# Performance work log

Measured on AMD Instinct MI355X. Metric: run time of the kernel, lower is better.

Reference implementation:

```python
import jax, jax.numpy as jnp
import numpy as np

N_HEADS = 16

def setup_inputs() -> dict:
    key = jax.random.key(0)
    ks = jax.random.split(key, 5)
    d = 2048
    s = 0.02
    return {
        "x": jax.random.normal(ks[0], (1, 2048, d), dtype=jnp.float32),
        "Wq": jax.random.normal(ks[1], (d, d), dtype=jnp.float32) * s,
        "bq": jnp.zeros((d,), jnp.float32),
        "Wk": jax.random.normal(ks[2], (d, d), dtype=jnp.float32) * s,
        "bk": jnp.zeros((d,), jnp.float32),
        "Wv": jax.random.normal(ks[3], (d, d), dtype=jnp.float32) * s,
        "bv": jnp.zeros((d,), jnp.float32),
        "Wo": jax.random.normal(ks[4], (d, d), dtype=jnp.float32) * s,
        "bo": jnp.zeros((d,), jnp.float32),
    }

def reference(x, Wq, bq, Wk, bk, Wv, bv, Wo, bo):
    B, S, D = x.shape
    H = N_HEADS
    dk = D // H
    # QKV projections -> [B, H, S, dk]
    def proj(W, b):
        return (x @ W + b).reshape(B, S, H, dk).transpose(0, 2, 1, 3)
    q, k, v = proj(Wq, bq), proj(Wk, bk), proj(Wv, bv)
    scores = jnp.einsum('bhqd,bhkd->bhqk', q, k) / jnp.sqrt(jnp.float32(dk))
    # _apply_sliding_window_attention: block-reshaped tril == plain causal mask
    causal = jnp.tril(jnp.ones((S, S), dtype=bool))
    scores = jnp.where(causal, scores, -jnp.inf)
    probs = jax.nn.softmax(scores, axis=-1)
    out = jnp.einsum('bhqk,bhkd->bhqd', probs, v)  # [B,H,S,dk]
    out = out.transpose(0, 2, 1, 3).reshape(B, S, D)
    return out @ Wo + bo
```

## Files before the change

kernel.cpp:

```cpp
#include <hip/hip_runtime.h>
#include <stdint.h>

typedef unsigned short u16;
typedef __attribute__((ext_vector_type(8))) __bf16 bf16x8;
typedef __attribute__((ext_vector_type(4))) float f32x4;

#define LOG2E 1.4426950408889634f

__device__ __forceinline__ u16 f2bf(float f) {
  union { float f; uint32_t u; } v; v.f = f;
  uint32_t r = v.u + 0x7fffu + ((v.u >> 16) & 1u);
  return (u16)(r >> 16);
}

__device__ __forceinline__ float bf2f(u16 u) {
  union { uint32_t u; float f; } v; v.u = ((uint32_t)u) << 16;
  return v.f;
}

__device__ __forceinline__ void gl_lds16(const void* g, void* l) {
  __builtin_amdgcn_global_load_lds((const __attribute__((address_space(1))) void*)g,
                                   (__attribute__((address_space(3))) void*)l,
                                   16, 0, 0);
}

__device__ __forceinline__ f32x4 mfma16(bf16x8 a, bf16x8 b, f32x4 c) {
  return __builtin_amdgcn_mfma_f32_16x16x32_bf16(a, b, c, 0, 0, 0);
}

__global__ void cvt_bf16(const float* __restrict__ src, u16* __restrict__ dst) {
  int i = (blockIdx.x * 256 + threadIdx.x) * 4;
  float4 f = *(const float4*)(src + i);
  ushort4 o;
  o.x = f2bf(f.x); o.y = f2bf(f.y); o.z = f2bf(f.z); o.w = f2bf(f.w);
  *(ushort4*)(dst + i) = o;
}

__global__ void transpose_cvt(const float* __restrict__ W0, const float* __restrict__ W1,
                              const float* __restrict__ W2, const float* __restrict__ W3,
                              u16* __restrict__ out) {
  __shared__ float tile[64][65];
  int z = blockIdx.z;
  const float* W = (z == 0) ? W0 : (z == 1) ? W1 : (z == 2) ? W2 : W3;
  u16* dst = out + (size_t)z * 2048 * 2048;
  int k0 = blockIdx.y * 64, n0 = blockIdx.x * 64;
  int lx = threadIdx.x & 63, ly = threadIdx.x >> 6;
#pragma unroll
  for (int p = 0; p < 16; ++p) {
    int row = p * 4 + ly;
    tile[row][lx] = W[(size_t)(k0 + row) * 2048 + n0 + lx];
  }
  __syncthreads();
#pragma unroll
  for (int p = 0; p < 16; ++p) {
    int row = p * 4 + ly;
    dst[(size_t)(n0 + row) * 2048 + k0 + lx] = f2bf(tile[lx][row]);
  }
}

__launch_bounds__(256, 2)
__global__ void gemm_bt(const u16* __restrict__ A, const u16* __restrict__ Bt,
                        int mode,
                        const float* __restrict__ b0, const float* __restrict__ b1,
                        const float* __restrict__ b2,
                        float* __restrict__ outF, u16* __restrict__ outQ,
                        u16* __restrict__ outK, u16* __restrict__ outVT) {
  extern __shared__ char smem[];
  u16* As = (u16*)smem;
  u16* Bs = (u16*)(smem + 16384);
  const int K = 2048;
  const int tid = threadIdx.x;
  const int lane = tid & 63, wid = tid >> 6;
  const int c = lane & 15, q = lane >> 4;
  const int wm = wid >> 1, wn = wid & 1;
  const int tm = blockIdx.y, tn = blockIdx.x;
  const size_t Abase = (size_t)tm * 128 * K;
  const size_t Bbase = (size_t)tn * 128 * K;

  f32x4 acc[4][4] = {};

  for (int kt = 0; kt < K / 64; ++kt) {
#pragma unroll
    for (int t = 0; t < 4; ++t) {
      int slot = wid * 256 + t * 64 + lane;
      int row = slot >> 3, cs = slot & 7;
      int cc = cs ^ (row & 7);
      const u16* ga = A + Abase + (size_t)row * K + kt * 64 + cc * 8;
      gl_lds16(ga, (char*)As + (size_t)(wid * 256 + t * 64) * 16);
      const u16* gb = Bt + Bbase + (size_t)row * K + kt * 64 + cc * 8;
      gl_lds16(gb, (char*)Bs + (size_t)(wid * 256 + t * 64) * 16);
    }
    __syncthreads();
#pragma unroll
    for (int kc = 0; kc < 2; ++kc) {
      bf16x8 af[4], bfr[4];
#pragma unroll
      for (int i = 0; i < 4; ++i) {
        int rowa = wm * 64 + i * 16 + c;
        int cha = ((kc << 2) | q) ^ (rowa & 7);
        af[i] = *(const bf16x8*)((const char*)As + rowa * 128 + cha * 16);
        int rowb = wn * 64 + i * 16 + c;
        int chb = ((kc << 2) | q) ^ (rowb & 7);
        bfr[i] = *(const bf16x8*)((const char*)Bs + rowb * 128 + chb * 16);
      }
#pragma unroll
      for (int i = 0; i < 4; ++i)
#pragma unroll
        for (int j = 0; j < 4; ++j)
          acc[i][j] = mfma16(af[i], bfr[j], acc[i][j]);
    }
    __syncthreads();
  }

  if (mode == 0) {
#pragma unroll
    for (int i = 0; i < 4; ++i) {
      int rowg = tm * 128 + wm * 64 + i * 16 + q * 4;
#pragma unroll
      for (int j = 0; j < 4; ++j) {
        int colg = tn * 128 + wn * 64 + j * 16 + c;
        float bias = b0[colg];
#pragma unroll
        for (int r = 0; r < 4; ++r)
          outF[(size_t)(rowg + r) * 2048 + colg] = acc[i][j][r] + bias;
      }
    }
  } else {
    int proj = tn >> 4;
    int h = tn & 15;
    const float* bias = (proj == 0) ? b0 : (proj == 1) ? b1 : b2;
    if (proj < 2) {
      u16* out = (proj == 0) ? outQ : outK;
      float scale = (proj == 0) ? 0.08838834764831845f : 1.0f;
#pragma unroll
      for (int i = 0; i < 4; ++i) {
        int s0 = tm * 128 + wm * 64 + i * 16 + q * 4;
#pragma unroll
        for (int j = 0; j < 4; ++j) {
          int d = wn * 64 + j * 16 + c;
          float bv = bias[h * 128 + d];
#pragma unroll
          for (int r = 0; r < 4; ++r) {
            float v = (acc[i][j][r] + bv) * scale;
            out[((size_t)h * 2048 + s0 + r) * 128 + d] = f2bf(v);
          }
        }
      }
    } else {
      u16* Cs = (u16*)smem;
#pragma unroll
      for (int i = 0; i < 4; ++i) {
        int sl = wm * 64 + i * 16 + q * 4;
#pragma unroll
        for (int j = 0; j < 4; ++j) {
          int dl = wn * 64 + j * 16 + c;
          float bv = bias[h * 128 + dl];
          ushort4 pk;
          pk.x = f2bf(acc[i][j][0] + bv);
          pk.y = f2bf(acc[i][j][1] + bv);
          pk.z = f2bf(acc[i][j][2] + bv);
          pk.w = f2bf(acc[i][j][3] + bv);
          *(ushort4*)(Cs + dl * 136 + sl) = pk;
        }
      }
      __syncthreads();
#pragma unroll
      for (int rr = 0; rr < 8; ++rr) {
        int d = rr * 16 + (tid >> 4);
        int sc = (tid & 15) * 8;
        uint4 vv = *(const uint4*)(Cs + d * 136 + sc);
        *(uint4*)(outVT + ((size_t)(h * 128 + d)) * 2048 + tm * 128 + sc) = vv;
      }
    }
  }
}

__launch_bounds__(256, 2)
__global__ void attn_kernel(const u16* __restrict__ Qb, const u16* __restrict__ Kb,
                            const u16* __restrict__ Vt,
                            u16* __restrict__ Op0, u16* __restrict__ Op1,
                            float* __restrict__ lp0, float* __restrict__ lp1) {
  extern __shared__ char smem[];
  u16* Ks = (u16*)smem;
  u16* Vs = (u16*)(smem + 16384);
  u16* Ps = (u16*)(smem + 32768);
  int b = blockIdx.x;
  int split, qt, h;
  if (b < 256) { split = 0; qt = b >> 4; h = b & 15; }
  else { split = 1; int idx = b - 256; qt = 15 - (idx >> 4); h = idx & 15; }
  u16* Op = split ? Op1 : Op0;
  float* lp = split ? lp1 : lp0;
  const int ktBase = split ? (qt + 1) : 0;
  const int ntiles = qt + 1;

  const int tid = threadIdx.x, lane = tid & 63, wid = tid >> 6;
  const int c = lane & 15, q = lane >> 4;

  bf16x8 qf[2][4];
#pragma unroll
  for (int i = 0; i < 2; ++i) {
    int s = qt * 128 + wid * 32 + i * 16 + c;
    const u16* qrow = Qb + ((size_t)h * 2048 + s) * 128;
#pragma unroll
    for (int kc = 0; kc < 4; ++kc)
      qf[i][kc] = *(const bf16x8*)(qrow + kc * 32 + q * 8);
  }

  f32x4 oacc[2][8] = {};
  float lst[2][4] = {};

  for (int tt = 0; tt < ntiles; ++tt) {
    const int kt = ktBase + tt;
    if (tt) __syncthreads();
#pragma unroll
    for (int t = 0; t < 4; ++t) {
      int slot = (wid * 4 + t) * 64 + lane;
      int rowk = slot >> 4, csk = slot & 15;
      int cck = csk ^ (rowk & 7);
      const u16* gk = Kb + ((size_t)h * 2048 + kt * 64 + rowk) * 128 + cck * 8;
      gl_lds16(gk, (char*)Ks + (size_t)((wid * 4 + t) * 64) * 16);
      int rowv = slot >> 3, csv = slot & 7;
      int ccv = csv ^ (rowv & 7);
      const u16* gv = Vt + ((size_t)(h * 128 + rowv)) * 2048 + kt * 64 + ccv * 8;
      gl_lds16(gv, (char*)Vs + (size_t)((wid * 4 + t) * 64) * 16);
    }
    __syncthreads();

    f32x4 sacc[2][4] = {};
#pragma unroll
    for (int kc = 0; kc < 4; ++kc) {
      bf16x8 bfr[4];
#pragma unroll
      for (int j = 0; j < 4; ++j) {
        int row = j * 16 + c;
        int ch = ((kc << 2) | q) ^ (row & 7);
        bfr[j] = *(const bf16x8*)((const char*)Ks + row * 256 + ch * 16);
      }
#pragma unroll
      for (int i = 0; i < 2; ++i)
#pragma unroll
        for (int j = 0; j < 4; ++j)
          sacc[i][j] = mfma16(qf[i][kc], bfr[j], sacc[i][j]);
    }

    if (kt >= 2 * qt) {
#pragma unroll
      for (int i = 0; i < 2; ++i)
#pragma unroll
        for (int j = 0; j < 4; ++j) {
          int key = kt * 64 + j * 16 + c;
#pragma unroll
          for (int r = 0; r < 4; ++r) {
            int qrow = qt * 128 + wid * 32 + i * 16 + q * 4 + r;
            if (key > qrow) sacc[i][j][r] = -1e30f;
          }
        }
    }

#pragma unroll
    for (int i = 0; i < 2; ++i)
#pragma unroll
      for (int j = 0; j < 4; ++j)
#pragma unroll
        for (int r = 0; r < 4; ++r) {
          float p = __builtin_amdgcn_exp2f(sacc[i][j][r] * LOG2E);
          sacc[i][j][r] = p;
          lst[i][r] += p;
        }

#pragma unroll
    for (int i = 0; i < 2; ++i)
#pragma unroll
      for (int j = 0; j < 4; ++j)
#pragma unroll
        for (int r = 0; r < 4; ++r)
          Ps[wid * 2304 + (i * 16 + q * 4 + r) * 72 + j * 16 + c] = f2bf(sacc[i][j][r]);

#pragma unroll
    for (int kc = 0; kc < 2; ++kc) {
      bf16x8 af[2], bv[8];
#pragma unroll
      for (int i = 0; i < 2; ++i)
        af[i] = *(const bf16x8*)((const char*)Ps + wid * 4608 + (i * 16 + c) * 144 +
                                 kc * 64 + q * 16);
#pragma unroll
      for (int jo = 0; jo < 8; ++jo) {
        int row = jo * 16 + c;
        int ch = ((kc << 2) | q) ^ (row & 7);
        bv[jo] = *(const bf16x8*)((const char*)Vs + row * 128 + ch * 16);
      }
#pragma unroll
      for (int i = 0; i < 2; ++i)
#pragma unroll
        for (int jo = 0; jo < 8; ++jo)
          oacc[i][jo] = mfma16(af[i], bv[jo], oacc[i][jo]);
    }
  }

#pragma unroll
  for (int i = 0; i < 2; ++i) {
#pragma unroll
    for (int r = 0; r < 4; ++r) {
      float l = lst[i][r];
      l += __shfl_xor(l, 1);
      l += __shfl_xor(l, 2);
      l += __shfl_xor(l, 4);
      l += __shfl_xor(l, 8);
      lst[i][r] = l;
      int s = qt * 128 + wid * 32 + i * 16 + q * 4 + r;
      if (c == 0) lp[(size_t)h * 2048 + s] = l;
    }
#pragma unroll
    for (int jo = 0; jo < 8; ++jo) {
#pragma unroll
      for (int r = 0; r < 4; ++r) {
        int s = qt * 128 + wid * 32 + i * 16 + q * 4 + r;
        Op[((size_t)h * 2048 + s) * 128 + jo * 16 + c] = f2bf(oacc[i][jo][r]);
      }
    }
  }
}

__global__ void attn_combine(const u16* __restrict__ Op0, const u16* __restrict__ Op1,
                             const float* __restrict__ lp0, const float* __restrict__ lp1,
                             u16* __restrict__ AO) {
  int g = blockIdx.x * 256 + threadIdx.x;
  int row = g >> 4;
  int dd = (g & 15) * 8;
  int h = row >> 11, s = row & 2047;
  float inv = 1.0f / (lp0[row] + lp1[row]);
  uint4 a = *(const uint4*)(Op0 + (size_t)row * 128 + dd);
  uint4 bb = *(const uint4*)(Op1 + (size_t)row * 128 + dd);
  const u16* pa = (const u16*)&a;
  const u16* pb = (const u16*)&bb;
  u16 res[8];
#pragma unroll
  for (int t = 0; t < 8; ++t)
    res[t] = f2bf((bf2f(pa[t]) + bf2f(pb[t])) * inv);
  *(uint4*)(AO + (size_t)s * 2048 + h * 128 + dd) = *(uint4*)res;
}

extern "C" void kernel_launch(void* const* d_in, const int* in_sizes, int n_in,
                              void* d_out, int out_size, void* d_ws, size_t ws_size,
                              hipStream_t stream) {
  const float* x  = (const float*)d_in[0];
  const float* Wq = (const float*)d_in[1];
  const float* bq = (const float*)d_in[2];
  const float* Wk = (const float*)d_in[3];
  const float* bk = (const float*)d_in[4];
  const float* Wv = (const float*)d_in[5];
  const float* bv = (const float*)d_in[6];
  const float* Wo = (const float*)d_in[7];
  const float* bo = (const float*)d_in[8];

  char* ws = (char*)d_ws;
  u16* xb = (u16*)(ws);
  u16* wt = (u16*)(ws + (size_t)8  * 1048576);
  u16* Qb = (u16*)(ws + (size_t)40 * 1048576);
  u16* Kb = (u16*)(ws + (size_t)48 * 1048576);
  u16* Vt = (u16*)(ws + (size_t)56 * 1048576);
  u16* AO = (u16*)(ws + (size_t)64 * 1048576);
  u16* Op0 = (u16*)(ws);
  u16* Op1 = (u16*)(ws + (size_t)8 * 1048576);
  float* l0 = (float*)(ws + (size_t)16 * 1048576);
  float* l1 = (float*)(ws + (size_t)16 * 1048576 + 131072);

  cvt_bf16<<<4096, 256, 0, stream>>>(x, xb);
  transpose_cvt<<<dim3(32, 32, 4), 256, 0, stream>>>(Wq, Wk, Wv, Wo, wt);
  gemm_bt<<<dim3(48, 16), 256, 34816, stream>>>(xb, wt, 1, bq, bk, bv,
                                                nullptr, Qb, Kb, Vt);
  attn_kernel<<<512, 256, 51200, stream>>>(Qb, Kb, Vt, Op0, Op1, l0, l1);
  attn_combine<<<2048, 256, 0, stream>>>(Op0, Op1, l0, l1, AO);
  gemm_bt<<<dim3(16, 16), 256, 34816, stream>>>(AO, wt + (size_t)3 * 2048 * 2048, 0,
                                                bo, nullptr, nullptr,
                                                (float*)d_out, nullptr, nullptr, nullptr);
}
```

Before: 264.4 us.

## Use packed bf16 conversion, vectorize stores, transpose PV MFMA, raise attention occupancy

Replaces the manual round-to-nearest bf16 conversion with the HIP packed float2-to-bfloat162 intrinsic, which can lower to a hardware packed-convert instruction on gfx950. Stores in the conversion, transpose and combine kernels are widened to 8- or 16-byte writes. In the attention kernel, the MFMA operands for the PV product are swapped so each lane holds four consecutive head-dim outputs, and the output is written as 8-byte vector stores. The attention kernel's launch bound is raised from 2 to 3 blocks per CU, which may force register spills.

```diff
diff --git a/kernel.cpp b/kernel.cpp
--- a/kernel.cpp
+++ b/kernel.cpp
@@ -1,4 +1,5 @@
 #include <hip/hip_runtime.h>
+#include <hip/hip_bf16.h>
 #include <stdint.h>
 
 typedef unsigned short u16;
@@ -7,15 +8,15 @@
 
 #define LOG2E 1.4426950408889634f
 
-__device__ __forceinline__ u16 f2bf(float f) {
-  union { float f; uint32_t u; } v; v.f = f;
-  uint32_t r = v.u + 0x7fffu + ((v.u >> 16) & 1u);
-  return (u16)(r >> 16);
-}
-
 __device__ __forceinline__ float bf2f(u16 u) {
   union { uint32_t u; float f; } v; v.u = ((uint32_t)u) << 16;
   return v.f;
+}
+
+__device__ __forceinline__ uint32_t pk2(float a, float b) {
+  union { __hip_bfloat162 h; uint32_t u; } x;
+  x.h = __float22bfloat162_rn(make_float2(a, b));
+  return x.u;
 }
 
 __device__ __forceinline__ void gl_lds16(const void* g, void* l) {
@@ -31,9 +32,10 @@
 __global__ void cvt_bf16(const float* __restrict__ src, u16* __restrict__ dst) {
   int i = (blockIdx.x * 256 + threadIdx.x) * 4;
   float4 f = *(const float4*)(src + i);
-  ushort4 o;
-  o.x = f2bf(f.x); o.y = f2bf(f.y); o.z = f2bf(f.z); o.w = f2bf(f.w);
-  *(ushort4*)(dst + i) = o;
+  uint2 o;
+  o.x = pk2(f.x, f.y);
+  o.y = pk2(f.z, f.w);
+  *(uint2*)(dst + i) = o;
 }
 
 __global__ void transpose_cvt(const float* __restrict__ W0, const float* __restrict__ W1,
@@ -51,10 +53,17 @@
     tile[row][lx] = W[(size_t)(k0 + row) * 2048 + n0 + lx];
   }
   __syncthreads();
-#pragma unroll
-  for (int p = 0; p < 16; ++p) {
-    int row = p * 4 + ly;
-    dst[(size_t)(n0 + row) * 2048 + k0 + lx] = f2bf(tile[lx][row]);
+  int kc = threadIdx.x & 7;
+  int rbase = threadIdx.x >> 3;
+#pragma unroll
+  for (int p = 0; p < 2; ++p) {
+    int n = rbase + p * 32;
+    uint4 o;
+    o.x = pk2(tile[kc * 8 + 0][n], tile[kc * 8 + 1][n]);
+    o.y = pk2(tile[kc * 8 + 2][n], tile[kc * 8 + 3][n]);
+    o.z = pk2(tile[kc * 8 + 4][n], tile[kc * 8 + 5][n]);
+    o.w = pk2(tile[kc * 8 + 6][n], tile[kc * 8 + 7][n]);
+    *(uint4*)(dst + (size_t)(n0 + n) * 2048 + k0 + kc * 8) = o;
   }
 }
 
@@ -139,11 +148,13 @@
         for (int j = 0; j < 4; ++j) {
           int d = wn * 64 + j * 16 + c;
           float bv = bias[h * 128 + d];
-#pragma unroll
-          for (int r = 0; r < 4; ++r) {
-            float v = (acc[i][j][r] + bv) * scale;
-            out[((size_t)h * 2048 + s0 + r) * 128 + d] = f2bf(v);
-          }
+          uint32_t p01 = pk2((acc[i][j][0] + bv) * scale, (acc[i][j][1] + bv) * scale);
+          uint32_t p23 = pk2((acc[i][j][2] + bv) * scale, (acc[i][j][3] + bv) * scale);
+          u16* o = out + ((size_t)h * 2048 + s0) * 128 + d;
+          o[0]       = (u16)p01;
+          o[128]     = (u16)(p01 >> 16);
+          o[256]     = (u16)p23;
+          o[384]     = (u16)(p23 >> 16);
         }
       }
     } else {
@@ -155,12 +166,10 @@
         for (int j = 0; j < 4; ++j) {
           int dl = wn * 64 + j * 16 + c;
           float bv = bias[h * 128 + dl];
-          ushort4 pk;
-          pk.x = f2bf(acc[i][j][0] + bv);
-          pk.y = f2bf(acc[i][j][1] + bv);
-          pk.z = f2bf(acc[i][j][2] + bv);
-          pk.w = f2bf(acc[i][j][3] + bv);
-          *(ushort4*)(Cs + dl * 136 + sl) = pk;
+          uint2 pk;
+          pk.x = pk2(acc[i][j][0] + bv, acc[i][j][1] + bv);
+          pk.y = pk2(acc[i][j][2] + bv, acc[i][j][3] + bv);
+          *(uint2*)(Cs + dl * 136 + sl) = pk;
         }
       }
       __syncthreads();
@@ -175,7 +184,7 @@
   }
 }
 
-__launch_bounds__(256, 2)
+__launch_bounds__(256, 3)
 __global__ void attn_kernel(const u16* __restrict__ Qb, const u16* __restrict__ Kb,
                             const u16* __restrict__ Vt,
                             u16* __restrict__ Op0, u16* __restrict__ Op1,
@@ -271,10 +280,15 @@
 #pragma unroll
     for (int i = 0; i < 2; ++i)
 #pragma unroll
-      for (int j = 0; j < 4; ++j)
-#pragma unroll
-        for (int r = 0; r < 4; ++r)
-          Ps[wid * 2304 + (i * 16 + q * 4 + r) * 72 + j * 16 + c] = f2bf(sacc[i][j][r]);
+      for (int j = 0; j < 4; ++j) {
+        uint32_t p01 = pk2(sacc[i][j][0], sacc[i][j][1]);
+        uint32_t p23 = pk2(sacc[i][j][2], sacc[i][j][3]);
+        u16* pp = Ps + wid * 2304 + (i * 16 + q * 4) * 72 + j * 16 + c;
+        pp[0]   = (u16)p01;
+        pp[72]  = (u16)(p01 >> 16);
+        pp[144] = (u16)p23;
+        pp[216] = (u16)(p23 >> 16);
+      }
 
 #pragma unroll
     for (int kc = 0; kc < 2; ++kc) {
@@ -293,12 +307,12 @@
       for (int i = 0; i < 2; ++i)
 #pragma unroll
         for (int jo = 0; jo < 8; ++jo)
-          oacc[i][jo] = mfma16(af[i], bv[jo], oacc[i][jo]);
-    }
-  }
-
-#pragma unroll
-  for (int i = 0; i < 2; ++i) {
+          oacc[i][jo] = mfma16(bv[jo], af[i], oacc[i][jo]);
+    }
+  }
+
+#pragma unroll
+  for (int i = 0; i < 2; ++i)
 #pragma unroll
     for (int r = 0; r < 4; ++r) {
       float l = lst[i][r];
@@ -306,17 +320,18 @@
       l += __shfl_xor(l, 2);
       l += __shfl_xor(l, 4);
       l += __shfl_xor(l, 8);
-      lst[i][r] = l;
-      int s = qt * 128 + wid * 32 + i * 16 + q * 4 + r;
-      if (c == 0) lp[(size_t)h * 2048 + s] = l;
-    }
+      if (c == 0)
+        lp[(size_t)h * 2048 + qt * 128 + wid * 32 + i * 16 + q * 4 + r] = l;
+    }
+#pragma unroll
+  for (int i = 0; i < 2; ++i) {
+    int s = qt * 128 + wid * 32 + i * 16 + c;
 #pragma unroll
     for (int jo = 0; jo < 8; ++jo) {
-#pragma unroll
-      for (int r = 0; r < 4; ++r) {
-        int s = qt * 128 + wid * 32 + i * 16 + q * 4 + r;
-        Op[((size_t)h * 2048 + s) * 128 + jo * 16 + c] = f2bf(oacc[i][jo][r]);
-      }
+      uint2 o;
+      o.x = pk2(oacc[i][jo][0], oacc[i][jo][1]);
+      o.y = pk2(oacc[i][jo][2], oacc[i][jo][3]);
+      *(uint2*)(Op + ((size_t)h * 2048 + s) * 128 + jo * 16 + q * 4) = o;
     }
   }
 }
@@ -333,11 +348,13 @@
   uint4 bb = *(const uint4*)(Op1 + (size_t)row * 128 + dd);
   const u16* pa = (const u16*)&a;
   const u16* pb = (const u16*)&bb;
-  u16 res[8];
-#pragma unroll
-  for (int t = 0; t < 8; ++t)
-    res[t] = f2bf((bf2f(pa[t]) + bf2f(pb[t])) * inv);
-  *(uint4*)(AO + (size_t)s * 2048 + h * 128 + dd) = *(uint4*)res;
+  uint4 res;
+  uint32_t* pr = (uint32_t*)&res;
+#pragma unroll
+  for (int t = 0; t < 4; ++t)
+    pr[t] = pk2((bf2f(pa[2 * t]) + bf2f(pb[2 * t])) * inv,
+                (bf2f(pa[2 * t + 1]) + bf2f(pb[2 * t + 1])) * inv);
+  *(uint4*)(AO + (size_t)s * 2048 + h * 128 + dd) = res;
 }
 
 extern "C" void kernel_launch(void* const* d_in, const int* in_sizes, int n_in,
```

Result: slower. 330.5 us (+25.0%).
